# Optimization experiments

Measured on AMD Instinct MI355X. Metric: run time of the kernel, lower is better.

## Reference

```python
import jax, jax.numpy as jnp
import numpy as np
from jax import lax

RATE = 0.3  # drop_rate from init_kwargs
B, L, E, U, V = 32, 64, 512, 512, 32000


def setup_inputs() -> dict:
    key = jax.random.key(0)
    ks = jax.random.split(key, 9)
    return {
        "pos_embs": jax.random.normal(ks[0], (B, L, E), jnp.float32),
        "images_emb": jax.random.normal(ks[1], (B, E), jnp.float32),
        "targets": jax.random.randint(ks[2], (B, L), 0, V, jnp.int64),
        # learned parameters
        "emb_table": jax.random.normal(ks[3], (V, E), jnp.float32) * 0.02,
        "W_in": jax.random.normal(ks[4], (E, 4 * U), jnp.float32) * 0.05,   # LSTM kernel (gate order i,f,c,o)
        "W_rec": jax.random.normal(ks[5], (U, 4 * U), jnp.float32) * 0.05,  # LSTM recurrent kernel
        "b_lstm": jnp.zeros((4 * U,), jnp.float32),
        "W_out": jax.random.normal(ks[6], (U, V), jnp.float32) * 0.02,
        "b_out": jnp.zeros((V,), jnp.float32),
    }


def _dropout_masks(batch, seq_len):
    """Deterministic dropout masks (training=True in the original)."""
    keep = 1.0 - RATE
    mk = jax.random.key(42)
    k1, k2, k3 = jax.random.split(mk, 3)
    # word dropout: noise_shape=(None,1,E) -> one mask per (batch, feature), shared over time
    word_mask = jax.random.bernoulli(k1, keep, (batch, 1, E)).astype(jnp.float32) / keep
    # Keras recurrent_dropout: 4 masks on h (one per gate), constant across timesteps
    rec_masks = jax.random.bernoulli(k2, keep, (4, batch, U)).astype(jnp.float32) / keep
    # final dropout on rnn_output [B, T, units]
    fin_mask = jax.random.bernoulli(k3, keep, (batch, seq_len, U)).astype(jnp.float32) / keep
    return word_mask, rec_masks, fin_mask


def reference(pos_embs, images_emb, targets, emb_table, W_in, W_rec, b_lstm, W_out, b_out):
    batch = pos_embs.shape[0]
    seq_len = targets.shape[1]  # (L-1) words + 1 image step = L
    word_mask, rec_masks, fin_mask = _dropout_masks(batch, seq_len)

    # embedding + word dropout (mask shared over time axis)
    word_embs = emb_table[targets[:, :-1]] * word_mask            # [B, L-1, E]
    x = jnp.concatenate([images_emb[:, None, :], word_embs], axis=1)  # [B, L, E]

    W_rec_g = W_rec.reshape(U, 4, U)  # [u, gate, u]

    def step(carry, x_t):
        h, c = carry
        z_in = x_t @ W_in + b_lstm                                # [B, 4U]
        # per-gate recurrent dropout on h, then recurrent matmul
        z_rec = jnp.einsum('gbu,ugv->bgv', h[None, :, :] * rec_masks, W_rec_g)
        z = z_in + z_rec.reshape(batch, 4 * U)
        zi, zf, zg, zo = jnp.split(z, 4, axis=-1)
        i = jax.nn.sigmoid(zi)
        f = jax.nn.sigmoid(zf)
        g = jnp.tanh(zg)
        o = jax.nn.sigmoid(zo)
        c_new = f * c + i * g
        h_new = o * jnp.tanh(c_new)
        return (h_new, c_new), h_new

    h0 = jnp.zeros((batch, U), x.dtype)
    (_, _), hs = lax.scan(step, (h0, h0), x.transpose(1, 0, 2))   # hs: [L, B, U]
    rnn_out = hs.transpose(1, 0, 2) * fin_mask                    # [B, L, U]

    predictions = rnn_out @ W_out + b_out                         # [B, L, V]
    return predictions
```

## Files before the change

### kernel.cpp

```cpp
#include <hip/hip_runtime.h>
#include <hip/hip_bf16.h>
#include <cstdint>
#include <cstddef>

struct TF2 { uint32_t a, b; };

__host__ __device__ constexpr uint32_t rotl32(uint32_t v, int r) {
  return (v << r) | (v >> (32 - r));
}

__host__ __device__ constexpr TF2 threefry2x32(uint32_t k0, uint32_t k1,
                                               uint32_t x0, uint32_t x1) {
  uint32_t ks0 = k0, ks1 = k1, ks2 = k0 ^ k1 ^ 0x1BD11BDAu;
  const int rotA[4] = {13, 15, 26, 6};
  const int rotB[4] = {17, 29, 16, 24};
  x0 += ks0; x1 += ks1;
  for (int i = 0; i < 5; ++i) {
    const int* rot = (i % 2 == 0) ? rotA : rotB;
    for (int j = 0; j < 4; ++j) {
      x0 += x1; x1 = rotl32(x1, rot[j]); x1 ^= x0;
    }
    uint32_t ks[3] = {ks0, ks1, ks2};
    x0 += ks[(i + 1) % 3];
    x1 += ks[(i + 2) % 3] + (uint32_t)(i + 1);
  }
  return TF2{x0, x1};
}

__device__ __forceinline__ float jax_mask(uint32_t child, uint32_t idx) {
  TF2 ck = threefry2x32(0u, 42u, 0u, child);
  TF2 r  = threefry2x32(ck.a, ck.b, 0u, idx);
  uint32_t bits = r.a ^ r.b;
  float u = __uint_as_float((bits >> 9) | 0x3f800000u) - 1.0f;
  return (u < 0.7f) ? (1.0f / 0.7f) : 0.0f;
}

__device__ __forceinline__ unsigned short f2bf(float f) {
  uint32_t u = __float_as_uint(f);
  uint32_t r = (u + 0x7fffu + ((u >> 16) & 1u)) >> 16;
  return (unsigned short)r;
}

typedef __attribute__((ext_vector_type(8))) short short8;
typedef __attribute__((ext_vector_type(4))) float f32x4;

__device__ __forceinline__ void async_copy16(const unsigned short* g, unsigned short* l) {
  __builtin_amdgcn_global_load_lds(
      (const __attribute__((address_space(1))) unsigned int*)g,
      (__attribute__((address_space(3))) unsigned int*)l, 16, 0, 0);
}

__global__ __launch_bounds__(256) void build_x_kernel(
    const float* __restrict__ img, const int* __restrict__ tgt,
    const float* __restrict__ emb, unsigned short* __restrict__ x) {
  const int idx = blockIdx.x * 256 + threadIdx.x;
  const int e = idx & 511;
  const int t = (idx >> 9) & 63;
  const int b = idx >> 15;
  float v;
  if (t == 0) {
    v = img[b * 512 + e];
  } else {
    const int w = tgt[b * 64 + (t - 1)];
    const float wm = jax_mask(0u, (uint32_t)(b * 512 + e));
    v = emb[(size_t)w * 512 + e] * wm;
  }
  x[idx] = f2bf(v);
}

__global__ __launch_bounds__(256) void rec_mask_kernel(float* __restrict__ rm) {
  const int idx = blockIdx.x * 256 + threadIdx.x;
  rm[idx] = jax_mask(1u, (uint32_t)idx);
}

__global__ __launch_bounds__(256) void transpose_wrec(
    const float* __restrict__ in, float* __restrict__ out) {
  __shared__ float tile[32][33];
  const int j0 = blockIdx.x * 32;
  const int u0 = blockIdx.y * 32;
  const int tx = threadIdx.x & 31;
  const int ty = threadIdx.x >> 5;
  for (int r = ty; r < 32; r += 8)
    tile[r][tx] = in[(size_t)(u0 + r) * 2048 + (j0 + tx)];
  __syncthreads();
  for (int r = ty; r < 32; r += 8)
    out[(size_t)(j0 + r) * 512 + (u0 + tx)] = tile[tx][r];
}

__global__ __launch_bounds__(256) void transpose_cvt(
    const float* __restrict__ in, unsigned short* __restrict__ out,
    int R, int C) {
  __shared__ float tile[32][33];
  const int c0 = blockIdx.x * 32;
  const int r0 = blockIdx.y * 32;
  const int tx = threadIdx.x & 31;
  const int ty = threadIdx.x >> 5;
  for (int r = ty; r < 32; r += 8)
    tile[r][tx] = in[(size_t)(r0 + r) * C + (c0 + tx)];
  __syncthreads();
  for (int r = ty; r < 32; r += 8)
    out[(size_t)(c0 + r) * R + (r0 + tx)] = f2bf(tile[tx][r]);
}

__global__ __launch_bounds__(256) void gemm_bf16_mfma(
    const unsigned short* __restrict__ A, const unsigned short* __restrict__ BT,
    const float* __restrict__ bias, float* __restrict__ C, int M, int N) {
  __shared__ unsigned short As[128 * 32];
  __shared__ unsigned short Bs[128 * 32];
  const int tid = threadIdx.x;
  const int lane = tid & 63;
  const int wave = tid >> 6;
  const int wm = (wave >> 1) * 64;
  const int wn = (wave & 1) * 64;
  const int m0 = blockIdx.y * 128;
  const int n0 = blockIdx.x * 128;

  f32x4 zero4 = {0.f, 0.f, 0.f, 0.f};
  f32x4 acc[4][4];
#pragma unroll
  for (int i = 0; i < 4; ++i)
#pragma unroll
    for (int j = 0; j < 4; ++j) acc[i][j] = zero4;

  const unsigned short* ga = A + (size_t)(m0 + (tid >> 2)) * 512 + (tid & 3) * 8;
  const unsigned short* gb = BT + (size_t)(n0 + (tid >> 2)) * 512 + (tid & 3) * 8;
  unsigned short* lwA = As + wave * 512;
  unsigned short* lwB = Bs + wave * 512;

  const int fr = lane & 15;
  const int kc = (lane >> 4) * 8;

  for (int k0 = 0; k0 < 512; k0 += 32) {
    __syncthreads();
    async_copy16(ga + k0, lwA);
    async_copy16(ga + k0 + 64 * 512, lwA + 2048);
    async_copy16(gb + k0, lwB);
    async_copy16(gb + k0 + 64 * 512, lwB + 2048);
    __syncthreads();

    short8 af[4], bf[4];
#pragma unroll
    for (int i = 0; i < 4; ++i)
      af[i] = *(const short8*)(As + (wm + i * 16 + fr) * 32 + kc);
#pragma unroll
    for (int i = 0; i < 4; ++i)
      bf[i] = *(const short8*)(Bs + (wn + i * 16 + fr) * 32 + kc);
#pragma unroll
    for (int mi = 0; mi < 4; ++mi)
#pragma unroll
      for (int ni = 0; ni < 4; ++ni)
        acc[mi][ni] = __builtin_amdgcn_mfma_f32_16x16x32_bf16(
            af[mi], bf[ni], acc[mi][ni], 0, 0, 0);
  }

#pragma unroll
  for (int mi = 0; mi < 4; ++mi) {
    const int mrow = m0 + wm + mi * 16 + (lane >> 4) * 4;
#pragma unroll
    for (int ni = 0; ni < 4; ++ni) {
      const int ncol = n0 + wn + ni * 16 + (lane & 15);
      const float bs = bias[ncol];
#pragma unroll
      for (int r2 = 0; r2 < 4; ++r2)
        C[(size_t)(mrow + r2) * N + ncol] = acc[mi][ni][r2] + bs;
    }
  }
}

__global__ __launch_bounds__(256) void lstm_step2(
    const float* __restrict__ zin, const float* __restrict__ WT,
    const float* __restrict__ rm, const float* __restrict__ hmr,
    float* __restrict__ hmw, float* __restrict__ c,
    unsigned short* __restrict__ rnn, const int t) {
  __shared__ __align__(16) float wl[32 * 132];
  __shared__ __align__(16) float hl[32 * 132];
  __shared__ float zsh[4][8][9];
  const int tid = threadIdx.x;
  const int u0 = (blockIdx.x & 63) * 8;
  const int b0 = (blockIdx.x >> 6) * 8;

  const int jl = tid & 31;
  const int bl = tid >> 5;
  const int g = jl >> 3, ul = jl & 7;
  const int b = b0 + bl;
  const float zv = zin[(size_t)(b * 64 + t) * 2048 + g * 512 + u0 + ul];

  const int srow = tid >> 3;
  const int sg = srow >> 3, sr = srow & 7;
  const float* wsrc = WT + (size_t)(sg * 512 + u0 + sr) * 512;
  const float* hsrc = hmr + (size_t)(sg * 32 + b0 + sr) * 512;

  const float4* wp = (const float4*)&wl[jl * 132];
  const float4* hp = (const float4*)&hl[(g * 8 + bl) * 132];

  float4 a0 = {0.f, 0.f, 0.f, 0.f}, a1 = {0.f, 0.f, 0.f, 0.f};

  for (int ph = 0; ph < 4; ++ph) {
    const int kbase = ph * 128;
    __syncthreads();
#pragma unroll
    for (int cc = 0; cc < 4; ++cc) {
      const int ch = (tid & 7) + cc * 8;
      *(float4*)&wl[srow * 132 + ch * 4] = *(const float4*)&wsrc[kbase + ch * 4];
      *(float4*)&hl[srow * 132 + ch * 4] = *(const float4*)&hsrc[kbase + ch * 4];
    }
    __syncthreads();
#pragma unroll 8
    for (int i = 0; i < 32; i += 2) {
      const float4 w0 = wp[i], h0 = hp[i];
      const float4 w1 = wp[i + 1], h1 = hp[i + 1];
      a0.x += w0.x * h0.x; a0.y += w0.y * h0.y;
      a0.z += w0.z * h0.z; a0.w += w0.w * h0.w;
      a1.x += w1.x * h1.x; a1.y += w1.y * h1.y;
      a1.z += w1.z * h1.z; a1.w += w1.w * h1.w;
    }
  }
  const float dot = (a0.x + a0.y + a0.z + a0.w) + (a1.x + a1.y + a1.z + a1.w);
  zsh[g][bl][ul] = zv + dot;
  __syncthreads();

  if (tid < 64) {
    const int uu = tid & 7, bb = tid >> 3;
    const float zi = zsh[0][bb][uu];
    const float zf = zsh[1][bb][uu];
    const float zg = zsh[2][bb][uu];
    const float zo = zsh[3][bb][uu];
    const float i_ = 1.f / (1.f + expf(-zi));
    const float f_ = 1.f / (1.f + expf(-zf));
    const float g_ = tanhf(zg);
    const float o_ = 1.f / (1.f + expf(-zo));
    const int bg = b0 + bb, ug = u0 + uu;
    const size_t cidx = (size_t)bg * 512 + ug;
    const float cn = f_ * c[cidx] + i_ * g_;
    c[cidx] = cn;
    const float hn = o_ * tanhf(cn);
    const float fm = jax_mask(2u, (uint32_t)((bg * 64 + t) * 512 + ug));
    rnn[(size_t)(bg * 64 + t) * 512 + ug] = f2bf(hn * fm);
#pragma unroll
    for (int gg = 0; gg < 4; ++gg) {
      const size_t o = (size_t)(gg * 32 + bg) * 512 + ug;
      hmw[o] = hn * rm[o];
    }
  }
}

extern "C" void kernel_launch(void* const* d_in, const int* in_sizes, int n_in,
                              void* d_out, int out_size, void* d_ws, size_t ws_size,
                              hipStream_t stream) {
  (void)in_sizes; (void)n_in; (void)out_size; (void)ws_size;
  const float* img   = (const float*)d_in[1];
  const int*   tgt   = (const int*)d_in[2];
  const float* emb   = (const float*)d_in[3];
  const float* W_in  = (const float*)d_in[4];
  const float* W_rec = (const float*)d_in[5];
  const float* b_l   = (const float*)d_in[6];
  const float* W_out = (const float*)d_in[7];
  const float* b_o   = (const float*)d_in[8];
  float* out = (float*)d_out;
  float* ws  = (float*)d_ws;

  float* zin = ws;
  float* WT  = ws + 4194304;
  float* hm0 = ws + 5242880;
  float* c   = ws + 5308416;
  float* hm1 = ws + 5324800;
  float* rm  = ws + 5390336;
  unsigned short* us = (unsigned short*)(ws + 5455872);
  unsigned short* x_bf  = us;
  unsigned short* WinT  = us + 1048576;
  unsigned short* rnn   = us + 2097152;
  unsigned short* WoutT = us + 3145728;

  hipMemsetAsync(hm0, 0, (size_t)(65536 + 16384) * sizeof(float), stream);

  build_x_kernel<<<4096, 256, 0, stream>>>(img, tgt, emb, x_bf);
  rec_mask_kernel<<<256, 256, 0, stream>>>(rm);
  transpose_wrec<<<dim3(64, 16), 256, 0, stream>>>(W_rec, WT);
  transpose_cvt<<<dim3(64, 16), 256, 0, stream>>>(W_in, WinT, 512, 2048);
  transpose_cvt<<<dim3(1000, 16), 256, 0, stream>>>(W_out, WoutT, 512, 32000);

  gemm_bf16_mfma<<<dim3(16, 16), 256, 0, stream>>>(x_bf, WinT, b_l, zin, 2048, 2048);

  for (int t = 0; t < 64; ++t) {
    const float* hr = (t & 1) ? hm1 : hm0;
    float*       hw = (t & 1) ? hm0 : hm1;
    lstm_step2<<<256, 256, 0, stream>>>(zin, WT, rm, hr, hw, c, rnn, t);
  }

  gemm_bf16_mfma<<<dim3(250, 16), 256, 0, stream>>>(rnn, WoutT, b_o, out, 2048, 32000);
}
```

Before: 1.089 ms.

## Replace per-timestep LSTM launches with persistent MFMA kernel and grid barrier

The 64 per-timestep launches of the fp32 recurrent kernel become one persistent 32-block kernel. Each block keeps its slice of W_rec in registers as split bf16 hi/lo pairs and computes the recurrent matmul with three MFMAs per step to keep near-fp32 accuracy. Timesteps are separated by an atomic-counter grid barrier with a spin guard, and the cell state stays in registers. The output GEMM grid is also swapped so M varies fastest, for better reuse of W_out tiles. The aim is to remove launch overhead and redundant weight reloads, at the cost of low parallelism (32 CUs), a spin barrier that needs every block resident at once, and approximation from the split-bf16 products.

Result: slower. 1.465 ms (+34.6%).

```diff
diff --git a/kernel.cpp b/kernel.cpp
--- a/kernel.cpp
+++ b/kernel.cpp
@@ -39,6 +39,9 @@
   uint32_t u = __float_as_uint(f);
   uint32_t r = (u + 0x7fffu + ((u >> 16) & 1u)) >> 16;
   return (unsigned short)r;
+}
+__device__ __forceinline__ float bf2f(unsigned short h) {
+  return __uint_as_float((uint32_t)h << 16);
 }
 
 typedef __attribute__((ext_vector_type(8))) short short8;
@@ -73,20 +76,6 @@
   rm[idx] = jax_mask(1u, (uint32_t)idx);
 }
 
-__global__ __launch_bounds__(256) void transpose_wrec(
-    const float* __restrict__ in, float* __restrict__ out) {
-  __shared__ float tile[32][33];
-  const int j0 = blockIdx.x * 32;
-  const int u0 = blockIdx.y * 32;
-  const int tx = threadIdx.x & 31;
-  const int ty = threadIdx.x >> 5;
-  for (int r = ty; r < 32; r += 8)
-    tile[r][tx] = in[(size_t)(u0 + r) * 2048 + (j0 + tx)];
-  __syncthreads();
-  for (int r = ty; r < 32; r += 8)
-    out[(size_t)(j0 + r) * 512 + (u0 + tx)] = tile[tx][r];
-}
-
 __global__ __launch_bounds__(256) void transpose_cvt(
     const float* __restrict__ in, unsigned short* __restrict__ out,
     int R, int C) {
@@ -102,6 +91,26 @@
     out[(size_t)(c0 + r) * R + (r0 + tx)] = f2bf(tile[tx][r]);
 }
 
+__global__ __launch_bounds__(256) void transpose_split(
+    const float* __restrict__ in, unsigned short* __restrict__ oh,
+    unsigned short* __restrict__ ol, int R, int C) {
+  __shared__ float tile[32][33];
+  const int c0 = blockIdx.x * 32;
+  const int r0 = blockIdx.y * 32;
+  const int tx = threadIdx.x & 31;
+  const int ty = threadIdx.x >> 5;
+  for (int r = ty; r < 32; r += 8)
+    tile[r][tx] = in[(size_t)(r0 + r) * C + (c0 + tx)];
+  __syncthreads();
+  for (int r = ty; r < 32; r += 8) {
+    const float v = tile[tx][r];
+    const unsigned short hi = f2bf(v);
+    const float lo = v - bf2f(hi);
+    oh[(size_t)(c0 + r) * R + (r0 + tx)] = hi;
+    ol[(size_t)(c0 + r) * R + (r0 + tx)] = f2bf(lo);
+  }
+}
+
 __global__ __launch_bounds__(256) void gemm_bf16_mfma(
     const unsigned short* __restrict__ A, const unsigned short* __restrict__ BT,
     const float* __restrict__ bias, float* __restrict__ C, int M, int N) {
@@ -112,8 +121,8 @@
   const int wave = tid >> 6;
   const int wm = (wave >> 1) * 64;
   const int wn = (wave & 1) * 64;
-  const int m0 = blockIdx.y * 128;
-  const int n0 = blockIdx.x * 128;
+  const int m0 = blockIdx.x * 128;
+  const int n0 = blockIdx.y * 128;
 
   f32x4 zero4 = {0.f, 0.f, 0.f, 0.f};
   f32x4 acc[4][4];
@@ -167,80 +176,113 @@
   }
 }
 
-__global__ __launch_bounds__(256) void lstm_step2(
-    const float* __restrict__ zin, const float* __restrict__ WT,
-    const float* __restrict__ rm, const float* __restrict__ hmr,
-    float* __restrict__ hmw, float* __restrict__ c,
-    unsigned short* __restrict__ rnn, const int t) {
-  __shared__ __align__(16) float wl[32 * 132];
-  __shared__ __align__(16) float hl[32 * 132];
-  __shared__ float zsh[4][8][9];
+#define LSTM_BLOCKS 32
+
+__global__ __launch_bounds__(256, 1) void lstm_persistent(
+    const float* __restrict__ zin, const unsigned short* __restrict__ WrTh,
+    const unsigned short* __restrict__ WrTl, const float* __restrict__ rm,
+    unsigned short* __restrict__ Abuf, unsigned short* __restrict__ rnn,
+    unsigned int* __restrict__ ctr) {
+  __shared__ float zsh[4][32][17];
   const int tid = threadIdx.x;
-  const int u0 = (blockIdx.x & 63) * 8;
-  const int b0 = (blockIdx.x >> 6) * 8;
-
-  const int jl = tid & 31;
-  const int bl = tid >> 5;
-  const int g = jl >> 3, ul = jl & 7;
-  const int b = b0 + bl;
-  const float zv = zin[(size_t)(b * 64 + t) * 2048 + g * 512 + u0 + ul];
-
-  const int srow = tid >> 3;
-  const int sg = srow >> 3, sr = srow & 7;
-  const float* wsrc = WT + (size_t)(sg * 512 + u0 + sr) * 512;
-  const float* hsrc = hmr + (size_t)(sg * 32 + b0 + sr) * 512;
-
-  const float4* wp = (const float4*)&wl[jl * 132];
-  const float4* hp = (const float4*)&hl[(g * 8 + bl) * 132];
-
-  float4 a0 = {0.f, 0.f, 0.f, 0.f}, a1 = {0.f, 0.f, 0.f, 0.f};
-
-  for (int ph = 0; ph < 4; ++ph) {
-    const int kbase = ph * 128;
-    __syncthreads();
-#pragma unroll
-    for (int cc = 0; cc < 4; ++cc) {
-      const int ch = (tid & 7) + cc * 8;
-      *(float4*)&wl[srow * 132 + ch * 4] = *(const float4*)&wsrc[kbase + ch * 4];
-      *(float4*)&hl[srow * 132 + ch * 4] = *(const float4*)&hsrc[kbase + ch * 4];
-    }
-    __syncthreads();
-#pragma unroll 8
-    for (int i = 0; i < 32; i += 2) {
-      const float4 w0 = wp[i], h0 = hp[i];
-      const float4 w1 = wp[i + 1], h1 = hp[i + 1];
-      a0.x += w0.x * h0.x; a0.y += w0.y * h0.y;
-      a0.z += w0.z * h0.z; a0.w += w0.w * h0.w;
-      a1.x += w1.x * h1.x; a1.y += w1.y * h1.y;
-      a1.z += w1.z * h1.z; a1.w += w1.w * h1.w;
-    }
-  }
-  const float dot = (a0.x + a0.y + a0.z + a0.w) + (a1.x + a1.y + a1.z + a1.w);
-  zsh[g][bl][ul] = zv + dot;
-  __syncthreads();
-
-  if (tid < 64) {
-    const int uu = tid & 7, bb = tid >> 3;
-    const float zi = zsh[0][bb][uu];
-    const float zf = zsh[1][bb][uu];
-    const float zg = zsh[2][bb][uu];
-    const float zo = zsh[3][bb][uu];
-    const float i_ = 1.f / (1.f + expf(-zi));
-    const float f_ = 1.f / (1.f + expf(-zf));
-    const float g_ = tanhf(zg);
-    const float o_ = 1.f / (1.f + expf(-zo));
-    const int bg = b0 + bb, ug = u0 + uu;
-    const size_t cidx = (size_t)bg * 512 + ug;
-    const float cn = f_ * c[cidx] + i_ * g_;
-    c[cidx] = cn;
-    const float hn = o_ * tanhf(cn);
-    const float fm = jax_mask(2u, (uint32_t)((bg * 64 + t) * 512 + ug));
-    rnn[(size_t)(bg * 64 + t) * 512 + ug] = f2bf(hn * fm);
-#pragma unroll
-    for (int gg = 0; gg < 4; ++gg) {
-      const size_t o = (size_t)(gg * 32 + bg) * 512 + ug;
-      hmw[o] = hn * rm[o];
-    }
+  const int g = tid >> 6;
+  const int lane = tid & 63;
+  const int fr = lane & 15;
+  const int kq = (lane >> 4) * 8;
+  const int u0 = blockIdx.x * 16;
+
+  short8 wh[16], wl[16];
+  {
+    const unsigned short* bph = WrTh + ((size_t)(g * 512 + u0 + fr) * 512 + kq);
+    const unsigned short* bpl = WrTl + ((size_t)(g * 512 + u0 + fr) * 512 + kq);
+#pragma unroll
+    for (int kk = 0; kk < 16; ++kk) {
+      wh[kk] = *(const short8*)(bph + kk * 32);
+      wl[kk] = *(const short8*)(bpl + kk * 32);
+    }
+  }
+
+  const int b_0 = tid >> 4;
+  const int ul = tid & 15;
+  const int u = u0 + ul;
+  float cst[2] = {0.f, 0.f};
+  float rmv[2][4];
+#pragma unroll
+  for (int gg = 0; gg < 4; ++gg) {
+    rmv[0][gg] = rm[(gg * 32 + b_0) * 512 + u];
+    rmv[1][gg] = rm[(gg * 32 + b_0 + 16) * 512 + u];
+  }
+
+  const size_t aoff = (size_t)(g * 32 + fr) * 512 + kq;
+
+  for (int t = 0; t < 64; ++t) {
+    const unsigned short* ar = Abuf + (size_t)(t & 1) * 131072;
+    unsigned short* aw = Abuf + (size_t)((t & 1) ^ 1) * 131072;
+
+    f32x4 acc0 = {0.f, 0.f, 0.f, 0.f};
+    f32x4 acc1 = {0.f, 0.f, 0.f, 0.f};
+#pragma unroll
+    for (int kk = 0; kk < 16; ++kk) {
+      const int off = kk * 32;
+      const short8 ah0 = *(const short8*)(ar + aoff + off);
+      const short8 al0 = *(const short8*)(ar + 65536 + aoff + off);
+      const short8 ah1 = *(const short8*)(ar + aoff + 16 * 512 + off);
+      const short8 al1 = *(const short8*)(ar + 65536 + aoff + 16 * 512 + off);
+      acc0 = __builtin_amdgcn_mfma_f32_16x16x32_bf16(ah0, wh[kk], acc0, 0, 0, 0);
+      acc0 = __builtin_amdgcn_mfma_f32_16x16x32_bf16(ah0, wl[kk], acc0, 0, 0, 0);
+      acc0 = __builtin_amdgcn_mfma_f32_16x16x32_bf16(al0, wh[kk], acc0, 0, 0, 0);
+      acc1 = __builtin_amdgcn_mfma_f32_16x16x32_bf16(ah1, wh[kk], acc1, 0, 0, 0);
+      acc1 = __builtin_amdgcn_mfma_f32_16x16x32_bf16(ah1, wl[kk], acc1, 0, 0, 0);
+      acc1 = __builtin_amdgcn_mfma_f32_16x16x32_bf16(al1, wh[kk], acc1, 0, 0, 0);
+    }
+    const int qm = (lane >> 4) * 4;
+#pragma unroll
+    for (int r = 0; r < 4; ++r) {
+      zsh[g][qm + r][fr] = acc0[r];
+      zsh[g][16 + qm + r][fr] = acc1[r];
+    }
+    __syncthreads();
+
+#pragma unroll
+    for (int half = 0; half < 2; ++half) {
+      const int b = b_0 + half * 16;
+      const float* zrow = zin + ((size_t)(b * 64 + t) * 2048 + u);
+      const float zi = zrow[0]    + zsh[0][b][ul];
+      const float zf = zrow[512]  + zsh[1][b][ul];
+      const float zg = zrow[1024] + zsh[2][b][ul];
+      const float zo = zrow[1536] + zsh[3][b][ul];
+      const float i_ = 1.f / (1.f + expf(-zi));
+      const float f_ = 1.f / (1.f + expf(-zf));
+      const float g_ = tanhf(zg);
+      const float o_ = 1.f / (1.f + expf(-zo));
+      const float cn = f_ * cst[half] + i_ * g_;
+      cst[half] = cn;
+      const float hn = o_ * tanhf(cn);
+      const float fm = jax_mask(2u, (uint32_t)((b * 64 + t) * 512 + u));
+      rnn[(size_t)(b * 64 + t) * 512 + u] = f2bf(hn * fm);
+#pragma unroll
+      for (int gg = 0; gg < 4; ++gg) {
+        const float hm = hn * rmv[half][gg];
+        const unsigned short hi = f2bf(hm);
+        const float lo = hm - bf2f(hi);
+        const size_t o = (size_t)(gg * 32 + b) * 512 + u;
+        aw[o] = hi;
+        aw[65536 + o] = f2bf(lo);
+      }
+    }
+
+    __threadfence();
+    __syncthreads();
+    if (tid == 0) {
+      __hip_atomic_fetch_add(ctr, 1u, __ATOMIC_ACQ_REL, __HIP_MEMORY_SCOPE_AGENT);
+      const unsigned int target = (unsigned int)(LSTM_BLOCKS * (t + 1));
+      long guard = 0;
+      while (__hip_atomic_load(ctr, __ATOMIC_ACQUIRE, __HIP_MEMORY_SCOPE_AGENT) < target) {
+        __builtin_amdgcn_s_sleep(2);
+        if (++guard > 400000000L) break;
+      }
+    }
+    __syncthreads();
   }
 }
 
@@ -260,32 +302,29 @@
   float* ws  = (float*)d_ws;
 
   float* zin = ws;
-  float* WT  = ws + 4194304;
-  float* hm0 = ws + 5242880;
-  float* c   = ws + 5308416;
-  float* hm1 = ws + 5324800;
-  float* rm  = ws + 5390336;
-  unsigned short* us = (unsigned short*)(ws + 5455872);
+  float* rm  = ws + 4194304;
+  unsigned int* ctr = (unsigned int*)(ws + 4259840);
+  unsigned short* us = (unsigned short*)(ws + 4259856);
   unsigned short* x_bf  = us;
   unsigned short* WinT  = us + 1048576;
   unsigned short* rnn   = us + 2097152;
-  unsigned short* WoutT = us + 3145728;
-
-  hipMemsetAsync(hm0, 0, (size_t)(65536 + 16384) * sizeof(float), stream);
+  unsigned short* WrTh  = us + 3145728;
+  unsigned short* WrTl  = us + 4194304;
+  unsigned short* Abuf  = us + 5242880;
+  unsigned short* WoutT = us + 5505024;
+
+  hipMemsetAsync(Abuf, 0, 131072 * sizeof(unsigned short), stream);
+  hipMemsetAsync(ctr, 0, 64, stream);
 
   build_x_kernel<<<4096, 256, 0, stream>>>(img, tgt, emb, x_bf);
   rec_mask_kernel<<<256, 256, 0, stream>>>(rm);
-  transpose_wrec<<<dim3(64, 16), 256, 0, stream>>>(W_rec, WT);
   transpose_cvt<<<dim3(64, 16), 256, 0, stream>>>(W_in, WinT, 512, 2048);
+  transpose_split<<<dim3(64, 16), 256, 0, stream>>>(W_rec, WrTh, WrTl, 512, 2048);
   transpose_cvt<<<dim3(1000, 16), 256, 0, stream>>>(W_out, WoutT, 512, 32000);
 
   gemm_bf16_mfma<<<dim3(16, 16), 256, 0, stream>>>(x_bf, WinT, b_l, zin, 2048, 2048);
 
-  for (int t = 0; t < 64; ++t) {
-    const float* hr = (t & 1) ? hm1 : hm0;
-    float*       hw = (t & 1) ? hm0 : hm1;
-    lstm_step2<<<256, 256, 0, stream>>>(zin, WT, rm, hr, hw, c, rnn, t);
-  }
-
-  gemm_bf16_mfma<<<dim3(250, 16), 256, 0, stream>>>(rnn, WoutT, b_o, out, 2048, 32000);
-}
+  lstm_persistent<<<LSTM_BLOCKS, 256, 0, stream>>>(zin, WrTh, WrTl, rm, Abuf, rnn, ctr);
+
+  gemm_bf16_mfma<<<dim3(16, 250), 256, 0, stream>>>(rnn, WoutT, b_o, out, 2048, 32000);
+}
```
